# Optimization experiments

Hardware: AMD Instinct MI355X
Metric: run time of the kernel (lower is better)

Reference implementation:

```python
import jax, jax.numpy as jnp
import numpy as np

H = 8  # num_heads
EPS = 1e-5


def layer_norm(x, g, b):
    mu = jnp.mean(x, axis=-1, keepdims=True)
    var = jnp.mean((x - mu) ** 2, axis=-1, keepdims=True)
    return (x - mu) * jax.lax.rsqrt(var + EPS) * g + b


def setup_inputs() -> dict:
    key = jax.random.key(0)
    ks = jax.random.split(key, 8)
    B, N, C = 2, 2048, 512
    Dff = 2048
    s = 0.02
    x = jax.random.normal(ks[0], (B, N, C), dtype=jnp.float32)
    mask = (jax.random.uniform(ks[1], (N, N)) > 0.5).astype(jnp.float32)
    return {
        "x": x,
        "mask": mask,
        "w_qkv": jax.random.normal(ks[2], (3 * C, C), dtype=jnp.float32) * s,
        "w_proj": jax.random.normal(ks[3], (C, C), dtype=jnp.float32) * s,
        "b_proj": jnp.zeros((C,), jnp.float32),
        "g1": jnp.ones((C,), jnp.float32),
        "beta1": jnp.zeros((C,), jnp.float32),
        "g2": jnp.ones((C,), jnp.float32),
        "beta2": jnp.zeros((C,), jnp.float32),
        "w1": jax.random.normal(ks[4], (Dff, C), dtype=jnp.float32) * s,
        "bm1": jnp.zeros((Dff,), jnp.float32),
        "w2": jax.random.normal(ks[5], (C, Dff), dtype=jnp.float32) * s,
        "bm2": jnp.zeros((C,), jnp.float32),
    }


def attn_block(h, mask, w_qkv, w_proj, b_proj):
    B, N, C = h.shape
    hd = C // H
    scale = hd ** -0.5
    qkv = (h @ w_qkv.T).reshape(B, N, 3, H, hd)
    q, k, v = jnp.moveaxis(qkv, 2, 0)          # each [B, N, H, hd]
    q = q.transpose(0, 2, 1, 3)                 # [B, H, N, hd]
    k = k.transpose(0, 2, 1, 3)
    v = v.transpose(0, 2, 1, 3)
    attn = jnp.einsum("bhnd,bhmd->bhnm", q, k) * scale
    attn = attn * mask                          # multiplicative sparse mask
    attn = jax.nn.softmax(attn, axis=-1)
    o = jnp.einsum("bhnm,bhmd->bhnd", attn, v)
    o = o.transpose(0, 2, 1, 3).reshape(B, N, C)
    return o @ w_proj.T + b_proj


def reference(x, mask, w_qkv, w_proj, b_proj, g1, beta1, g2, beta2, w1, bm1, w2, bm2):
    # pre-norm transformer block, dropout/drop_path disabled (eval)
    y = x + attn_block(layer_norm(x, g1, beta1), mask, w_qkv, w_proj, b_proj)
    h = layer_norm(y, g2, beta2)
    h = jax.nn.gelu(h @ w1.T + bm1, approximate=False)  # torch F.gelu default (erf)
    z = y + (h @ w2.T + bm2)
    return z
```

## Files before the change

kernel.cpp:

```cpp
#include <hip/hip_runtime.h>
#include <cmath>
#include <stdint.h>

#define N_SEQ 2048
#define C_DIM 512
#define BATCH 2
#define NHEAD 8
#define DFF   2048
#define M_ROWS (BATCH * N_SEQ)

typedef unsigned short ushort_t;
typedef unsigned long long u64;
typedef __bf16 bf16x8 __attribute__((ext_vector_type(8)));
typedef float  f32x4  __attribute__((ext_vector_type(4)));
typedef float  f32x16 __attribute__((ext_vector_type(16)));

__device__ __forceinline__ float bf2f(ushort_t u) {
    union { unsigned int i; float f; } v; v.i = ((unsigned int)u) << 16; return v.f;
}
__device__ __forceinline__ ushort_t f2bf_(float f) {
    union { float f; unsigned int i; } v; v.f = f;
    unsigned int r = v.i + 0x7fffu + ((v.i >> 16) & 1u);
    return (ushort_t)(r >> 16);
}
__device__ __forceinline__ unsigned short bfbits(float f) {
    return __builtin_bit_cast(unsigned short, (__bf16)f);
}

__device__ __forceinline__ void load_lds16(const ushort_t* g, ushort_t* lds_wave_base) {
    __builtin_amdgcn_global_load_lds(
        (const __attribute__((address_space(1))) void*)g,
        (__attribute__((address_space(3))) void*)lds_wave_base, 16, 0, 0);
}

__global__ void probe_kernel(const unsigned int* __restrict__ g1w, int* __restrict__ flag) {
    if (threadIdx.x == 0 && blockIdx.x == 0)
        *flag = (g1w[0] == 0x3F800000u) ? 1 : 0;
}

__global__ __launch_bounds__(256) void convert_kernel(const int* __restrict__ flag,
        const void* w_qkv, const void* w_proj, const void* w1, const void* w2,
        ushort_t* wq_bf, ushort_t* wp_bf, ushort_t* w1_bf, ushort_t* w2_bf) {
    long e = ((long)blockIdx.x * 256 + threadIdx.x) * 8;
    const void* src; ushort_t* dst; long off;
    if      (e < 786432)  { src = w_qkv; dst = wq_bf;  off = e; }
    else if (e < 1048576) { src = w_proj; dst = wp_bf; off = e - 786432; }
    else if (e < 2097152) { src = w1;    dst = w1_bf;  off = e - 1048576; }
    else                  { src = w2;    dst = w2_bf;  off = e - 2097152; }
    bf16x8 r;
    if (*flag) {
        const float4* q = (const float4*)((const float*)src + off);
        float4 a = q[0], b = q[1];
        r[0]=(__bf16)a.x; r[1]=(__bf16)a.y; r[2]=(__bf16)a.z; r[3]=(__bf16)a.w;
        r[4]=(__bf16)b.x; r[5]=(__bf16)b.y; r[6]=(__bf16)b.z; r[7]=(__bf16)b.w;
    } else {
        r = *(const bf16x8*)((const ushort_t*)src + off);
    }
    *(bf16x8*)(dst + off) = r;
}

__global__ __launch_bounds__(256) void maskpack_kernel(const int* __restrict__ flag,
        const void* __restrict__ mask, u64* __restrict__ maskM) {
    int id = blockIdx.x * 256 + threadIdx.x;
    int q = id >> 5, kb = id & 31;
    int is32 = *flag;
    size_t base = (size_t)q * N_SEQ + kb * 64;
    u64 bits = 0;
    for (int j = 0; j < 64; ++j) {
        bool m = is32 ? (((const float*)mask)[base + j] != 0.0f)
                      : ((((const ushort_t*)mask)[base + j] & 0x7fffu) != 0);
        bits |= (u64)m << j;
    }
    maskM[(size_t)q * 32 + kb] = bits;
}

template <typename TX, typename TG>
__device__ __forceinline__ void ln_body(const TX* __restrict__ x, const TG* __restrict__ g,
                                        const TG* __restrict__ b, ushort_t* __restrict__ out) {
    int row  = blockIdx.x * 4 + (threadIdx.x >> 6);
    int lane = threadIdx.x & 63;
    const TX* xr = x + (size_t)row * C_DIM + lane * 8;
    float v[8];
    if (sizeof(TX) == 2) {
        bf16x8 t = *(const bf16x8*)xr;
        #pragma unroll
        for (int j = 0; j < 8; ++j) v[j] = (float)t[j];
    } else {
        const float4* q = (const float4*)xr;
        float4 a = q[0], c = q[1];
        v[0]=a.x; v[1]=a.y; v[2]=a.z; v[3]=a.w; v[4]=c.x; v[5]=c.y; v[6]=c.z; v[7]=c.w;
    }
    float s = 0.f, sq = 0.f;
    #pragma unroll
    for (int j = 0; j < 8; ++j) { s += v[j]; sq += v[j] * v[j]; }
    #pragma unroll
    for (int m = 1; m < 64; m <<= 1) { s += __shfl_xor(s, m, 64); sq += __shfl_xor(sq, m, 64); }
    float mean = s * (1.0f / C_DIM);
    float var  = fmaxf(sq * (1.0f / C_DIM) - mean * mean, 0.0f);
    float rs = rsqrtf(var + 1e-5f);
    float gv[8], bv[8];
    const TG* gp = g + lane * 8; const TG* bp = b + lane * 8;
    if (sizeof(TG) == 2) {
        bf16x8 tg = *(const bf16x8*)gp, tb = *(const bf16x8*)bp;
        #pragma unroll
        for (int j = 0; j < 8; ++j) { gv[j] = (float)tg[j]; bv[j] = (float)tb[j]; }
    } else {
        const float4* qg = (const float4*)gp; const float4* qb = (const float4*)bp;
        float4 a=qg[0], c=qg[1], d=qb[0], e=qb[1];
        gv[0]=a.x;gv[1]=a.y;gv[2]=a.z;gv[3]=a.w;gv[4]=c.x;gv[5]=c.y;gv[6]=c.z;gv[7]=c.w;
        bv[0]=d.x;bv[1]=d.y;bv[2]=d.z;bv[3]=d.w;bv[4]=e.x;bv[5]=e.y;bv[6]=e.z;bv[7]=e.w;
    }
    bf16x8 o;
    #pragma unroll
    for (int j = 0; j < 8; ++j) o[j] = (__bf16)((v[j] - mean) * rs * gv[j] + bv[j]);
    *(bf16x8*)(out + (size_t)row * C_DIM + lane * 8) = o;
}

__global__ __launch_bounds__(256) void ln1_kernel(const int* __restrict__ flag, const void* x,
                                                  const void* g, const void* b, ushort_t* out) {
    if (*flag) ln_body<float, float>((const float*)x, (const float*)g, (const float*)b, out);
    else       ln_body<ushort_t, ushort_t>((const ushort_t*)x, (const ushort_t*)g, (const ushort_t*)b, out);
}
__global__ __launch_bounds__(256) void ln2_kernel(const int* __restrict__ flag, const ushort_t* y,
                                                  const void* g, const void* b, ushort_t* out) {
    if (*flag) ln_body<ushort_t, float>(y, (const float*)g, (const float*)b, out);
    else       ln_body<ushort_t, ushort_t>(y, (const ushort_t*)g, (const ushort_t*)b, out);
}

template <int BN, int K, bool HAS_BIAS, int ACT, int RES_MODE, int OUT_MODE>
__global__ __launch_bounds__(256) void gemm_kernel(const int* __restrict__ flag,
        const ushort_t* __restrict__ A, const ushort_t* __restrict__ W,
        const void* __restrict__ bias, const void* __restrict__ res,
        void* __restrict__ Cout, int Nout) {
    constexpr int MT  = (BN == 128) ? 2 : 1;
    constexpr int RPW = (BN == 128) ? 32 : 16;
    __shared__ __align__(16) ushort_t As[64 * 32];
    __shared__ __align__(16) ushort_t Bs[BN * 32];
    int t = threadIdx.x;
    int wave = t >> 6, lane = t & 63, quad = lane >> 4, l16 = lane & 15;
    int wm = (BN == 128) ? (wave >> 1) : wave;
    int wn = (BN == 128) ? (wave & 1) : 0;
    int row0 = blockIdx.y * 64, col0 = blockIdx.x * BN;

    f32x4 acc[MT][4] = {};
    int arow = t >> 2, kofs = (t & 3) * 8;

    for (int k0 = 0; k0 < K; k0 += 32) {
        load_lds16(A + (size_t)(row0 + arow) * K + k0 + kofs, As + wave * 512);
        load_lds16(W + (size_t)(col0 + arow) * K + k0 + kofs, Bs + wave * 512);
        if (BN == 128)
            load_lds16(W + (size_t)(col0 + 64 + arow) * K + k0 + kofs, Bs + 2048 + wave * 512);
        __syncthreads();
        bf16x8 af[MT], bfr[4];
        #pragma unroll
        for (int i = 0; i < MT; ++i)
            af[i] = *(const bf16x8*)&As[(wm * RPW + i * 16 + l16) * 32 + quad * 8];
        #pragma unroll
        for (int j = 0; j < 4; ++j)
            bfr[j] = *(const bf16x8*)&Bs[(wn * 64 + j * 16 + l16) * 32 + quad * 8];
        #pragma unroll
        for (int i = 0; i < MT; ++i)
            #pragma unroll
            for (int j = 0; j < 4; ++j)
                acc[i][j] = __builtin_amdgcn_mfma_f32_16x16x32_bf16(af[i], bfr[j], acc[i][j], 0, 0, 0);
        __syncthreads();
    }

    int is32 = *flag;
    #pragma unroll
    for (int j = 0; j < 4; ++j) {
        int col = col0 + wn * 64 + j * 16 + l16;
        float bv = 0.0f;
        if (HAS_BIAS) bv = is32 ? ((const float*)bias)[col] : bf2f(((const ushort_t*)bias)[col]);
        #pragma unroll
        for (int i = 0; i < MT; ++i) {
            #pragma unroll
            for (int r = 0; r < 4; ++r) {
                int row = row0 + wm * RPW + i * 16 + quad * 4 + r;
                float v = acc[i][j][r] + bv;
                if (ACT == 1) v = 0.5f * v * (1.0f + erff(v * 0.70710678118654752f));
                size_t idx = (size_t)row * Nout + col;
                if (RES_MODE == 1) v += is32 ? ((const float*)res)[idx] : bf2f(((const ushort_t*)res)[idx]);
                if (RES_MODE == 3) v += bf2f(((const ushort_t*)res)[idx]);
                if (OUT_MODE == 0) ((ushort_t*)Cout)[idx] = f2bf_(v);
                else { if (is32) ((float*)Cout)[idx] = v; else ((ushort_t*)Cout)[idx] = f2bf_(v); }
            }
        }
    }
}

__global__ __launch_bounds__(128) void attn_kernel(
        const ushort_t* __restrict__ qkv, const u64* __restrict__ maskM,
        ushort_t* __restrict__ o0, ushort_t* __restrict__ o1,
        ushort_t* __restrict__ o2, ushort_t* __restrict__ o3,
        float* __restrict__ Lpart) {
    __shared__ __align__(16) ushort_t Ks[64][68];
    __shared__ __align__(16) ushort_t VTs[64][68];
    int t = threadIdx.x;
    int wave = t >> 6, lane = t & 63, l32 = lane & 31, H = lane >> 5;
    int qtile = blockIdx.x, bh = blockIdx.y, sp = blockIdx.z;
    int b = bh >> 3, h = bh & 7;
    int q = qtile * 64 + wave * 32 + l32;

    const ushort_t* base = qkv + (size_t)b * N_SEQ * 1536;
    const ushort_t* qp = base + h * 64;
    const ushort_t* kp = base + 512 + h * 64;
    const ushort_t* vp = base + 1024 + h * 64;

    bf16x8 bQ[4];
    #pragma unroll
    for (int c = 0; c < 4; ++c)
        bQ[c] = *(const bf16x8*)(qp + (size_t)q * 1536 + c * 16 + H * 8);

    int k_row = (t >> 3);
    int k_ch  = (t & 7) * 8;
    int v_kp0 = (t & 31) * 2;
    int v_db0 = (t >> 5) * 8;
    const int n_base = sp * 512;

    bf16x8 kreg[4], vreg[2][2];
    #pragma unroll
    for (int s = 0; s < 4; ++s)
        kreg[s] = *(const bf16x8*)(kp + (size_t)(n_base + s * 16 + k_row) * 1536 + k_ch);
    #pragma unroll
    for (int s = 0; s < 2; ++s)
        #pragma unroll
        for (int u = 0; u < 2; ++u)
            vreg[s][u] = *(const bf16x8*)(vp + (size_t)(n_base + v_kp0 + u) * 1536 + v_db0 + s * 32);
    u64 mw = maskM[(size_t)q * 32 + (n_base >> 6)];

    f32x16 o_acc[2] = {};
    float lsum = 0.0f;
    const float scale = 0.125f;

    for (int i = 0; i < 8; ++i) {
        int n0 = n_base + i * 64;
        __syncthreads();
        #pragma unroll
        for (int s = 0; s < 4; ++s)
            *(bf16x8*)&Ks[s * 16 + k_row][k_ch] = kreg[s];
        #pragma unroll
        for (int s = 0; s < 2; ++s)
            #pragma unroll
            for (int j = 0; j < 8; ++j) {
                unsigned int pair = (unsigned int)__builtin_bit_cast(unsigned short, vreg[s][0][j])
                                  | ((unsigned int)__builtin_bit_cast(unsigned short, vreg[s][1][j]) << 16);
                *(unsigned int*)&VTs[v_db0 + s * 32 + j][v_kp0] = pair;
            }
        __syncthreads();
        if (i < 7) {
            int n1 = n0 + 64;
            #pragma unroll
            for (int s = 0; s < 4; ++s)
                kreg[s] = *(const bf16x8*)(kp + (size_t)(n1 + s * 16 + k_row) * 1536 + k_ch);
            #pragma unroll
            for (int s = 0; s < 2; ++s)
                #pragma unroll
                for (int u = 0; u < 2; ++u)
                    vreg[s][u] = *(const bf16x8*)(vp + (size_t)(n1 + v_kp0 + u) * 1536 + v_db0 + s * 32);
        }
        f32x16 s_acc[2] = {};
        #pragma unroll
        for (int kt = 0; kt < 2; ++kt)
            #pragma unroll
            for (int c = 0; c < 4; ++c) {
                bf16x8 aK = *(const bf16x8*)&Ks[kt * 32 + l32][c * 16 + H * 8];
                s_acc[kt] = __builtin_amdgcn_mfma_f32_32x32x16_bf16(aK, bQ[c], s_acc[kt], 0, 0, 0);
            }
        unsigned int P2[2][8];
        #pragma unroll
        for (int kt = 0; kt < 2; ++kt) {
            float p[16];
            #pragma unroll
            for (int r = 0; r < 16; ++r) {
                int keyloc = kt * 32 + (r & 3) + 8 * (r >> 2) + 4 * H;
                float e = __expf(s_acc[kt][r] * scale);
                p[r] = ((mw >> keyloc) & 1) ? e : 1.0f;
                lsum += p[r];
            }
            #pragma unroll
            for (int pr = 0; pr < 8; ++pr)
                P2[kt][pr] = (unsigned int)bfbits(p[2 * pr])
                           | ((unsigned int)bfbits(p[2 * pr + 1]) << 16);
        }
        if (i < 7) mw = maskM[(size_t)q * 32 + ((n0 + 64) >> 6)];
        unsigned int rv[2][4];
        #pragma unroll
        for (int kt = 0; kt < 2; ++kt)
            #pragma unroll
            for (int u = 0; u < 4; ++u) {
                int idx = (u & 1) + (u >> 1) * 4;
                unsigned int send = H ? P2[kt][idx] : P2[kt][idx + 2];
                rv[kt][u] = (unsigned int)__shfl_xor((int)send, 32, 64);
            }
        #pragma unroll
        for (int kc = 0; kc < 4; ++kc) {
            const int kt = kc >> 1, klo = kc & 1;
            union { unsigned int w[4]; bf16x8 v; } bP;
            #pragma unroll
            for (int w = 0; w < 4; ++w) {
                unsigned int own = H ? P2[kt][(w & 1) + 4 * klo + 2] : P2[kt][(w & 1) + 4 * klo];
                unsigned int oth = rv[kt][(w & 1) + 2 * klo];
                bP.w[w] = ((w >> 1) == H) ? own : oth;
            }
            #pragma unroll
            for (int dt = 0; dt < 2; ++dt) {
                bf16x8 aV = *(const bf16x8*)&VTs[dt * 32 + l32][kc * 16 + H * 8];
                o_acc[dt] = __builtin_amdgcn_mfma_f32_32x32x16_bf16(aV, bP.v, o_acc[dt], 0, 0, 0);
            }
        }
    }
    lsum += __shfl_xor(lsum, 32, 64);
    ushort_t* osel = (sp == 0) ? o0 : (sp == 1) ? o1 : (sp == 2) ? o2 : o3;
    ushort_t* op = osel + (size_t)bh * N_SEQ * 64;
    #pragma unroll
    for (int dt = 0; dt < 2; ++dt)
        #pragma unroll
        for (int r4 = 0; r4 < 4; ++r4) {
            int d = dt * 32 + 8 * r4 + 4 * H;
            ushort4 val;
            val.x = f2bf_(o_acc[dt][r4 * 4 + 0]);
            val.y = f2bf_(o_acc[dt][r4 * 4 + 1]);
            val.z = f2bf_(o_acc[dt][r4 * 4 + 2]);
            val.w = f2bf_(o_acc[dt][r4 * 4 + 3]);
            *(ushort4*)&op[(size_t)q * 64 + d] = val;
        }
    if (H == 0)
        Lpart[((size_t)sp * 16 + bh) * N_SEQ + q] = lsum;
}

__global__ __launch_bounds__(256) void combine_kernel(
        const ushort_t* __restrict__ o0, const ushort_t* __restrict__ o1,
        const ushort_t* __restrict__ o2, const ushort_t* __restrict__ o3,
        const float* __restrict__ Lpart, ushort_t* __restrict__ attno) {
    int gid = blockIdx.x * 256 + threadIdx.x;
    int rowg = gid >> 4;
    int dq = (gid & 15) * 4;
    int bh = rowg >> 11, qq = rowg & 2047, b = bh >> 3, h = bh & 7;
    const ushort_t* ops[4] = { o0, o1, o2, o3 };
    float acc[4] = {};
    float l = 0.0f;
    #pragma unroll
    for (int sp = 0; sp < 4; ++sp) {
        ushort4 o = *(const ushort4*)&ops[sp][(size_t)rowg * 64 + dq];
        acc[0] += bf2f(o.x); acc[1] += bf2f(o.y); acc[2] += bf2f(o.z); acc[3] += bf2f(o.w);
        l += Lpart[(size_t)sp * 16 * N_SEQ + rowg];
    }
    float inv = 1.0f / l;
    ushort4 res;
    res.x = f2bf_(acc[0] * inv); res.y = f2bf_(acc[1] * inv);
    res.z = f2bf_(acc[2] * inv); res.w = f2bf_(acc[3] * inv);
    *(ushort4*)&attno[((size_t)b * N_SEQ + qq) * C_DIM + h * 64 + dq] = res;
}

extern "C" void kernel_launch(void* const* d_in, const int* in_sizes, int n_in,
                              void* d_out, int out_size, void* d_ws, size_t ws_size,
                              hipStream_t stream) {
    char* ws = (char*)d_ws;
    const size_t KB = 1024;
    int*      flag  = (int*)ws;
    ushort_t* wq_bf = (ushort_t*)(ws + 256 * KB);
    ushort_t* wp_bf = (ushort_t*)(ws + 1792 * KB);
    ushort_t* w1_bf = (ushort_t*)(ws + 2304 * KB);
    ushort_t* w2_bf = (ushort_t*)(ws + 4352 * KB);
    u64*      maskM = (u64*)     (ws + 6400 * KB);
    ushort_t* h     = (ushort_t*)(ws + 6912 * KB);
    ushort_t* attno = (ushort_t*)(ws + 11008 * KB);
    ushort_t* y     = (ushort_t*)(ws + 15104 * KB);
    ushort_t* qkv   = (ushort_t*)(ws + 19200 * KB);
    ushort_t* Op2   = (ushort_t*)(ws + 31488 * KB);
    ushort_t* Op3   = (ushort_t*)(ws + 35584 * KB);
    float*    Lpart = (float*)   (ws + 39680 * KB);
    ushort_t* Op0   = h;
    ushort_t* Op1   = y;
    ushort_t* gmid  = (ushort_t*)(ws + 19200 * KB);

    probe_kernel<<<1, 64, 0, stream>>>((const unsigned int*)d_in[5], flag);
    convert_kernel<<<1536, 256, 0, stream>>>(flag, d_in[2], d_in[3], d_in[9], d_in[11],
                                             wq_bf, wp_bf, w1_bf, w2_bf);
    maskpack_kernel<<<256, 256, 0, stream>>>(flag, d_in[1], maskM);
    ln1_kernel<<<M_ROWS / 4, 256, 0, stream>>>(flag, d_in[0], d_in[5], d_in[6], h);
    gemm_kernel<128, 512, false, 0, 0, 0><<<dim3(1536 / 128, 64), 256, 0, stream>>>(
        flag, h, wq_bf, nullptr, nullptr, qkv, 1536);
    attn_kernel<<<dim3(N_SEQ / 64, BATCH * NHEAD, 4), 128, 0, stream>>>(
        qkv, maskM, Op0, Op1, Op2, Op3, Lpart);
    combine_kernel<<<2048, 256, 0, stream>>>(Op0, Op1, Op2, Op3, Lpart, attno);
    gemm_kernel<64, 512, true, 0, 1, 0><<<dim3(C_DIM / 64, 64), 256, 0, stream>>>(
        flag, attno, wp_bf, d_in[4], d_in[0], y, C_DIM);
    ln2_kernel<<<M_ROWS / 4, 256, 0, stream>>>(flag, y, d_in[7], d_in[8], h);
    gemm_kernel<128, 512, true, 1, 0, 0><<<dim3(DFF / 128, 64), 256, 0, stream>>>(
        flag, h, w1_bf, d_in[10], nullptr, gmid, DFF);
    gemm_kernel<64, 2048, true, 0, 3, 2><<<dim3(C_DIM / 64, 64), 256, 0, stream>>>(
        flag, gmid, w2_bf, d_in[12], y, d_out, C_DIM);
}
```

Baseline: 263.1 us.

## Fuse prep kernels, fold split-K combine into proj GEMM, enlarge attention tiles

Merges the probe, weight convert, mask pack and LN1 kernels into one prep launch, and packs the mask with wave ballots instead of a serial per-thread loop. The split-attention combine moves into the projection GEMM's A-tile load, which removes the intermediate attno buffer and a launch. The attention kernel now runs 256 threads per block over 128 queries, and pre-scales Q by scale*log2e so it can use exp2f. The costs are redundant partial-sum and reciprocal work on every K-step of the proj GEMM, and a register-staged A load in place of the direct global-to-LDS load.

Measured after the change: 352.8 us. 34.1% more time.

```diff
diff --git a/kernel.cpp b/kernel.cpp
--- a/kernel.cpp
+++ b/kernel.cpp
@@ -26,6 +26,9 @@
 __device__ __forceinline__ unsigned short bfbits(float f) {
     return __builtin_bit_cast(unsigned short, (__bf16)f);
 }
+__device__ __forceinline__ int get_is32(const unsigned int* g1w) {
+    return g1w[0] == 0x3F800000u;
+}
 
 __device__ __forceinline__ void load_lds16(const ushort_t* g, ushort_t* lds_wave_base) {
     __builtin_amdgcn_global_load_lds(
@@ -33,52 +36,10 @@
         (__attribute__((address_space(3))) void*)lds_wave_base, 16, 0, 0);
 }
 
-__global__ void probe_kernel(const unsigned int* __restrict__ g1w, int* __restrict__ flag) {
-    if (threadIdx.x == 0 && blockIdx.x == 0)
-        *flag = (g1w[0] == 0x3F800000u) ? 1 : 0;
-}
-
-__global__ __launch_bounds__(256) void convert_kernel(const int* __restrict__ flag,
-        const void* w_qkv, const void* w_proj, const void* w1, const void* w2,
-        ushort_t* wq_bf, ushort_t* wp_bf, ushort_t* w1_bf, ushort_t* w2_bf) {
-    long e = ((long)blockIdx.x * 256 + threadIdx.x) * 8;
-    const void* src; ushort_t* dst; long off;
-    if      (e < 786432)  { src = w_qkv; dst = wq_bf;  off = e; }
-    else if (e < 1048576) { src = w_proj; dst = wp_bf; off = e - 786432; }
-    else if (e < 2097152) { src = w1;    dst = w1_bf;  off = e - 1048576; }
-    else                  { src = w2;    dst = w2_bf;  off = e - 2097152; }
-    bf16x8 r;
-    if (*flag) {
-        const float4* q = (const float4*)((const float*)src + off);
-        float4 a = q[0], b = q[1];
-        r[0]=(__bf16)a.x; r[1]=(__bf16)a.y; r[2]=(__bf16)a.z; r[3]=(__bf16)a.w;
-        r[4]=(__bf16)b.x; r[5]=(__bf16)b.y; r[6]=(__bf16)b.z; r[7]=(__bf16)b.w;
-    } else {
-        r = *(const bf16x8*)((const ushort_t*)src + off);
-    }
-    *(bf16x8*)(dst + off) = r;
-}
-
-__global__ __launch_bounds__(256) void maskpack_kernel(const int* __restrict__ flag,
-        const void* __restrict__ mask, u64* __restrict__ maskM) {
-    int id = blockIdx.x * 256 + threadIdx.x;
-    int q = id >> 5, kb = id & 31;
-    int is32 = *flag;
-    size_t base = (size_t)q * N_SEQ + kb * 64;
-    u64 bits = 0;
-    for (int j = 0; j < 64; ++j) {
-        bool m = is32 ? (((const float*)mask)[base + j] != 0.0f)
-                      : ((((const ushort_t*)mask)[base + j] & 0x7fffu) != 0);
-        bits |= (u64)m << j;
-    }
-    maskM[(size_t)q * 32 + kb] = bits;
-}
-
 template <typename TX, typename TG>
-__device__ __forceinline__ void ln_body(const TX* __restrict__ x, const TG* __restrict__ g,
-                                        const TG* __restrict__ b, ushort_t* __restrict__ out) {
-    int row  = blockIdx.x * 4 + (threadIdx.x >> 6);
-    int lane = threadIdx.x & 63;
+__device__ __forceinline__ void ln_row(int row, int lane, const TX* __restrict__ x,
+                                       const TG* __restrict__ g, const TG* __restrict__ b,
+                                       ushort_t* __restrict__ out) {
     const TX* xr = x + (size_t)row * C_DIM + lane * 8;
     float v[8];
     if (sizeof(TX) == 2) {
@@ -116,19 +77,59 @@
     *(bf16x8*)(out + (size_t)row * C_DIM + lane * 8) = o;
 }
 
-__global__ __launch_bounds__(256) void ln1_kernel(const int* __restrict__ flag, const void* x,
-                                                  const void* g, const void* b, ushort_t* out) {
-    if (*flag) ln_body<float, float>((const float*)x, (const float*)g, (const float*)b, out);
-    else       ln_body<ushort_t, ushort_t>((const ushort_t*)x, (const ushort_t*)g, (const ushort_t*)b, out);
-}
-__global__ __launch_bounds__(256) void ln2_kernel(const int* __restrict__ flag, const ushort_t* y,
-                                                  const void* g, const void* b, ushort_t* out) {
-    if (*flag) ln_body<ushort_t, float>(y, (const float*)g, (const float*)b, out);
-    else       ln_body<ushort_t, ushort_t>(y, (const ushort_t*)g, (const ushort_t*)b, out);
+__global__ __launch_bounds__(256) void prep_kernel(const unsigned int* __restrict__ g1w,
+        const void* w_qkv, const void* w_proj, const void* w1, const void* w2,
+        const void* mask, const void* x, const void* g1, const void* b1,
+        ushort_t* wq_bf, ushort_t* wp_bf, ushort_t* w1_bf, ushort_t* w2_bf,
+        u64* __restrict__ maskM, ushort_t* __restrict__ hout) {
+    int is32 = get_is32(g1w);
+    int bid = blockIdx.x;
+    int wave = threadIdx.x >> 6, lane = threadIdx.x & 63;
+    if (bid < 1536) {
+        long e = ((long)bid * 256 + threadIdx.x) * 8;
+        const void* src; ushort_t* dst; long off;
+        if      (e < 786432)  { src = w_qkv; dst = wq_bf;  off = e; }
+        else if (e < 1048576) { src = w_proj; dst = wp_bf; off = e - 786432; }
+        else if (e < 2097152) { src = w1;    dst = w1_bf;  off = e - 1048576; }
+        else                  { src = w2;    dst = w2_bf;  off = e - 2097152; }
+        bf16x8 r;
+        if (is32) {
+            const float4* q = (const float4*)((const float*)src + off);
+            float4 a = q[0], b = q[1];
+            r[0]=(__bf16)a.x; r[1]=(__bf16)a.y; r[2]=(__bf16)a.z; r[3]=(__bf16)a.w;
+            r[4]=(__bf16)b.x; r[5]=(__bf16)b.y; r[6]=(__bf16)b.z; r[7]=(__bf16)b.w;
+        } else {
+            r = *(const bf16x8*)((const ushort_t*)src + off);
+        }
+        *(bf16x8*)(dst + off) = r;
+    } else if (bid < 2560) {
+        int pb = bid - 1536;
+        #pragma unroll
+        for (int it = 0; it < 16; ++it) {
+            int p = pb * 64 + wave * 16 + it;
+            int q = p >> 5, kb = p & 31;
+            size_t idx = (size_t)q * N_SEQ + kb * 64 + lane;
+            bool m = is32 ? (((const float*)mask)[idx] != 0.0f)
+                          : ((((const ushort_t*)mask)[idx] & 0x7fffu) != 0);
+            u64 bits = __ballot(m);
+            if (lane == 0) maskM[(size_t)q * 32 + kb] = bits;
+        }
+    } else {
+        int row = (bid - 2560) * 4 + wave;
+        if (is32) ln_row<float, float>(row, lane, (const float*)x, (const float*)g1, (const float*)b1, hout);
+        else      ln_row<ushort_t, ushort_t>(row, lane, (const ushort_t*)x, (const ushort_t*)g1, (const ushort_t*)b1, hout);
+    }
+}
+
+__global__ __launch_bounds__(256) void ln2_kernel(const unsigned int* __restrict__ g1w,
+        const ushort_t* __restrict__ y, const void* g, const void* b, ushort_t* out) {
+    int row = blockIdx.x * 4 + (threadIdx.x >> 6), lane = threadIdx.x & 63;
+    if (get_is32(g1w)) ln_row<ushort_t, float>(row, lane, y, (const float*)g, (const float*)b, out);
+    else               ln_row<ushort_t, ushort_t>(row, lane, y, (const ushort_t*)g, (const ushort_t*)b, out);
 }
 
 template <int BN, int K, bool HAS_BIAS, int ACT, int RES_MODE, int OUT_MODE>
-__global__ __launch_bounds__(256) void gemm_kernel(const int* __restrict__ flag,
+__global__ __launch_bounds__(256) void gemm_kernel(const unsigned int* __restrict__ g1w,
         const ushort_t* __restrict__ A, const ushort_t* __restrict__ W,
         const void* __restrict__ bias, const void* __restrict__ res,
         void* __restrict__ Cout, int Nout) {
@@ -166,7 +167,7 @@
         __syncthreads();
     }
 
-    int is32 = *flag;
+    int is32 = get_is32(g1w);
     #pragma unroll
     for (int j = 0; j < 4; ++j) {
         int col = col0 + wn * 64 + j * 16 + l16;
@@ -180,7 +181,6 @@
                 float v = acc[i][j][r] + bv;
                 if (ACT == 1) v = 0.5f * v * (1.0f + erff(v * 0.70710678118654752f));
                 size_t idx = (size_t)row * Nout + col;
-                if (RES_MODE == 1) v += is32 ? ((const float*)res)[idx] : bf2f(((const ushort_t*)res)[idx]);
                 if (RES_MODE == 3) v += bf2f(((const ushort_t*)res)[idx]);
                 if (OUT_MODE == 0) ((ushort_t*)Cout)[idx] = f2bf_(v);
                 else { if (is32) ((float*)Cout)[idx] = v; else ((ushort_t*)Cout)[idx] = f2bf_(v); }
@@ -189,7 +189,68 @@
     }
 }
 
-__global__ __launch_bounds__(128) void attn_kernel(
+__global__ __launch_bounds__(256) void proj_gemm_kernel(const unsigned int* __restrict__ g1w,
+        const ushort_t* __restrict__ o0, const ushort_t* __restrict__ o1,
+        const ushort_t* __restrict__ o2, const ushort_t* __restrict__ o3,
+        const float* __restrict__ Lpart,
+        const ushort_t* __restrict__ W, const void* __restrict__ bias,
+        const void* __restrict__ res, ushort_t* __restrict__ Cout) {
+    __shared__ __align__(16) ushort_t As[64 * 32];
+    __shared__ __align__(16) ushort_t Bs[64 * 32];
+    int t = threadIdx.x;
+    int wave = t >> 6, lane = t & 63, quad = lane >> 4, l16 = lane & 15;
+    int row0 = blockIdx.y * 64, col0 = blockIdx.x * 64;
+
+    f32x4 acc[4] = {};
+    int arow = t >> 2, kofs = (t & 3) * 8;
+    int row_t = row0 + arow;
+    int b_ = row_t >> 11, q_ = row_t & 2047;
+
+    for (int k0 = 0; k0 < 512; k0 += 32) {
+        int k = k0 + kofs;
+        int hh = k >> 6, d = k & 63;
+        size_t rowg = (size_t)(b_ * 8 + hh) * 2048 + q_;
+        float l = Lpart[rowg] + Lpart[32768 + rowg] + Lpart[65536 + rowg] + Lpart[98304 + rowg];
+        float inv = 1.0f / l;
+        const ushort_t* p0 = o0 + rowg * 64 + d;
+        const ushort_t* p1 = o1 + rowg * 64 + d;
+        const ushort_t* p2 = o2 + rowg * 64 + d;
+        const ushort_t* p3 = o3 + rowg * 64 + d;
+        bf16x8 av;
+        #pragma unroll
+        for (int j = 0; j < 8; ++j) {
+            float s = bf2f(p0[j]) + bf2f(p1[j]) + bf2f(p2[j]) + bf2f(p3[j]);
+            av[j] = (__bf16)(s * inv);
+        }
+        *(bf16x8*)&As[arow * 32 + kofs] = av;
+        load_lds16(W + (size_t)(col0 + arow) * 512 + k0 + kofs, Bs + wave * 512);
+        __syncthreads();
+        bf16x8 af = *(const bf16x8*)&As[(wave * 16 + l16) * 32 + quad * 8];
+        #pragma unroll
+        for (int j = 0; j < 4; ++j) {
+            bf16x8 bfr = *(const bf16x8*)&Bs[(j * 16 + l16) * 32 + quad * 8];
+            acc[j] = __builtin_amdgcn_mfma_f32_16x16x32_bf16(af, bfr, acc[j], 0, 0, 0);
+        }
+        __syncthreads();
+    }
+
+    int is32 = get_is32(g1w);
+    #pragma unroll
+    for (int j = 0; j < 4; ++j) {
+        int col = col0 + j * 16 + l16;
+        float bv = is32 ? ((const float*)bias)[col] : bf2f(((const ushort_t*)bias)[col]);
+        #pragma unroll
+        for (int r = 0; r < 4; ++r) {
+            int row = row0 + wave * 16 + quad * 4 + r;
+            size_t idx = (size_t)row * C_DIM + col;
+            float v = acc[j][r] + bv;
+            v += is32 ? ((const float*)res)[idx] : bf2f(((const ushort_t*)res)[idx]);
+            Cout[idx] = f2bf_(v);
+        }
+    }
+}
+
+__global__ __launch_bounds__(256, 4) void attn_kernel(
         const ushort_t* __restrict__ qkv, const u64* __restrict__ maskM,
         ushort_t* __restrict__ o0, ushort_t* __restrict__ o1,
         ushort_t* __restrict__ o2, ushort_t* __restrict__ o3,
@@ -200,64 +261,59 @@
     int wave = t >> 6, lane = t & 63, l32 = lane & 31, H = lane >> 5;
     int qtile = blockIdx.x, bh = blockIdx.y, sp = blockIdx.z;
     int b = bh >> 3, h = bh & 7;
-    int q = qtile * 64 + wave * 32 + l32;
+    int q = qtile * 128 + wave * 32 + l32;
 
     const ushort_t* base = qkv + (size_t)b * N_SEQ * 1536;
     const ushort_t* qp = base + h * 64;
     const ushort_t* kp = base + 512 + h * 64;
     const ushort_t* vp = base + 1024 + h * 64;
 
+    const float qs = 0.125f * 1.44269504088896f;
     bf16x8 bQ[4];
     #pragma unroll
-    for (int c = 0; c < 4; ++c)
-        bQ[c] = *(const bf16x8*)(qp + (size_t)q * 1536 + c * 16 + H * 8);
-
-    int k_row = (t >> 3);
-    int k_ch  = (t & 7) * 8;
-    int v_kp0 = (t & 31) * 2;
-    int v_db0 = (t >> 5) * 8;
+    for (int c = 0; c < 4; ++c) {
+        bf16x8 raw = *(const bf16x8*)(qp + (size_t)q * 1536 + c * 16 + H * 8);
+        #pragma unroll
+        for (int j = 0; j < 8; ++j) bQ[c][j] = (__bf16)((float)raw[j] * qs);
+    }
+
+    int k_r = t >> 3, k_ch = (t & 7) * 8;
+    int v_kp = (t & 31) * 2, v_db = (t >> 5) * 8;
     const int n_base = sp * 512;
 
-    bf16x8 kreg[4], vreg[2][2];
-    #pragma unroll
-    for (int s = 0; s < 4; ++s)
-        kreg[s] = *(const bf16x8*)(kp + (size_t)(n_base + s * 16 + k_row) * 1536 + k_ch);
+    bf16x8 kreg[2], vreg[2];
     #pragma unroll
     for (int s = 0; s < 2; ++s)
-        #pragma unroll
-        for (int u = 0; u < 2; ++u)
-            vreg[s][u] = *(const bf16x8*)(vp + (size_t)(n_base + v_kp0 + u) * 1536 + v_db0 + s * 32);
+        kreg[s] = *(const bf16x8*)(kp + (size_t)(n_base + s * 32 + k_r) * 1536 + k_ch);
+    #pragma unroll
+    for (int u = 0; u < 2; ++u)
+        vreg[u] = *(const bf16x8*)(vp + (size_t)(n_base + v_kp + u) * 1536 + v_db);
     u64 mw = maskM[(size_t)q * 32 + (n_base >> 6)];
 
     f32x16 o_acc[2] = {};
     float lsum = 0.0f;
-    const float scale = 0.125f;
 
     for (int i = 0; i < 8; ++i) {
         int n0 = n_base + i * 64;
         __syncthreads();
         #pragma unroll
-        for (int s = 0; s < 4; ++s)
-            *(bf16x8*)&Ks[s * 16 + k_row][k_ch] = kreg[s];
-        #pragma unroll
         for (int s = 0; s < 2; ++s)
-            #pragma unroll
-            for (int j = 0; j < 8; ++j) {
-                unsigned int pair = (unsigned int)__builtin_bit_cast(unsigned short, vreg[s][0][j])
-                                  | ((unsigned int)__builtin_bit_cast(unsigned short, vreg[s][1][j]) << 16);
-                *(unsigned int*)&VTs[v_db0 + s * 32 + j][v_kp0] = pair;
-            }
+            *(bf16x8*)&Ks[s * 32 + k_r][k_ch] = kreg[s];
+        #pragma unroll
+        for (int j = 0; j < 8; ++j) {
+            unsigned int pair = (unsigned int)__builtin_bit_cast(unsigned short, vreg[0][j])
+                              | ((unsigned int)__builtin_bit_cast(unsigned short, vreg[1][j]) << 16);
+            *(unsigned int*)&VTs[v_db + j][v_kp] = pair;
+        }
         __syncthreads();
         if (i < 7) {
             int n1 = n0 + 64;
             #pragma unroll
-            for (int s = 0; s < 4; ++s)
-                kreg[s] = *(const bf16x8*)(kp + (size_t)(n1 + s * 16 + k_row) * 1536 + k_ch);
-            #pragma unroll
             for (int s = 0; s < 2; ++s)
-                #pragma unroll
-                for (int u = 0; u < 2; ++u)
-                    vreg[s][u] = *(const bf16x8*)(vp + (size_t)(n1 + v_kp0 + u) * 1536 + v_db0 + s * 32);
+                kreg[s] = *(const bf16x8*)(kp + (size_t)(n1 + s * 32 + k_r) * 1536 + k_ch);
+            #pragma unroll
+            for (int u = 0; u < 2; ++u)
+                vreg[u] = *(const bf16x8*)(vp + (size_t)(n1 + v_kp + u) * 1536 + v_db);
         }
         f32x16 s_acc[2] = {};
         #pragma unroll
@@ -274,7 +330,7 @@
             #pragma unroll
             for (int r = 0; r < 16; ++r) {
                 int keyloc = kt * 32 + (r & 3) + 8 * (r >> 2) + 4 * H;
-                float e = __expf(s_acc[kt][r] * scale);
+                float e = exp2f(s_acc[kt][r]);
                 p[r] = ((mw >> keyloc) & 1) ? e : 1.0f;
                 lsum += p[r];
             }
@@ -329,67 +385,39 @@
         Lpart[((size_t)sp * 16 + bh) * N_SEQ + q] = lsum;
 }
 
-__global__ __launch_bounds__(256) void combine_kernel(
-        const ushort_t* __restrict__ o0, const ushort_t* __restrict__ o1,
-        const ushort_t* __restrict__ o2, const ushort_t* __restrict__ o3,
-        const float* __restrict__ Lpart, ushort_t* __restrict__ attno) {
-    int gid = blockIdx.x * 256 + threadIdx.x;
-    int rowg = gid >> 4;
-    int dq = (gid & 15) * 4;
-    int bh = rowg >> 11, qq = rowg & 2047, b = bh >> 3, h = bh & 7;
-    const ushort_t* ops[4] = { o0, o1, o2, o3 };
-    float acc[4] = {};
-    float l = 0.0f;
-    #pragma unroll
-    for (int sp = 0; sp < 4; ++sp) {
-        ushort4 o = *(const ushort4*)&ops[sp][(size_t)rowg * 64 + dq];
-        acc[0] += bf2f(o.x); acc[1] += bf2f(o.y); acc[2] += bf2f(o.z); acc[3] += bf2f(o.w);
-        l += Lpart[(size_t)sp * 16 * N_SEQ + rowg];
-    }
-    float inv = 1.0f / l;
-    ushort4 res;
-    res.x = f2bf_(acc[0] * inv); res.y = f2bf_(acc[1] * inv);
-    res.z = f2bf_(acc[2] * inv); res.w = f2bf_(acc[3] * inv);
-    *(ushort4*)&attno[((size_t)b * N_SEQ + qq) * C_DIM + h * 64 + dq] = res;
-}
-
 extern "C" void kernel_launch(void* const* d_in, const int* in_sizes, int n_in,
                               void* d_out, int out_size, void* d_ws, size_t ws_size,
                               hipStream_t stream) {
     char* ws = (char*)d_ws;
     const size_t KB = 1024;
-    int*      flag  = (int*)ws;
-    ushort_t* wq_bf = (ushort_t*)(ws + 256 * KB);
-    ushort_t* wp_bf = (ushort_t*)(ws + 1792 * KB);
-    ushort_t* w1_bf = (ushort_t*)(ws + 2304 * KB);
-    ushort_t* w2_bf = (ushort_t*)(ws + 4352 * KB);
-    u64*      maskM = (u64*)     (ws + 6400 * KB);
-    ushort_t* h     = (ushort_t*)(ws + 6912 * KB);
-    ushort_t* attno = (ushort_t*)(ws + 11008 * KB);
-    ushort_t* y     = (ushort_t*)(ws + 15104 * KB);
-    ushort_t* qkv   = (ushort_t*)(ws + 19200 * KB);
-    ushort_t* Op2   = (ushort_t*)(ws + 31488 * KB);
-    ushort_t* Op3   = (ushort_t*)(ws + 35584 * KB);
-    float*    Lpart = (float*)   (ws + 39680 * KB);
-    ushort_t* Op0   = h;
-    ushort_t* Op1   = y;
-    ushort_t* gmid  = (ushort_t*)(ws + 19200 * KB);
-
-    probe_kernel<<<1, 64, 0, stream>>>((const unsigned int*)d_in[5], flag);
-    convert_kernel<<<1536, 256, 0, stream>>>(flag, d_in[2], d_in[3], d_in[9], d_in[11],
-                                             wq_bf, wp_bf, w1_bf, w2_bf);
-    maskpack_kernel<<<256, 256, 0, stream>>>(flag, d_in[1], maskM);
-    ln1_kernel<<<M_ROWS / 4, 256, 0, stream>>>(flag, d_in[0], d_in[5], d_in[6], h);
+    const unsigned int* g1w = (const unsigned int*)d_in[5];
+    ushort_t* wq_bf = (ushort_t*)(ws);
+    ushort_t* wp_bf = (ushort_t*)(ws + 1536 * KB);
+    ushort_t* w1_bf = (ushort_t*)(ws + 2048 * KB);
+    ushort_t* w2_bf = (ushort_t*)(ws + 4096 * KB);
+    u64*      maskM = (u64*)     (ws + 6144 * KB);
+    ushort_t* h     = (ushort_t*)(ws + 6656 * KB);
+    ushort_t* y     = (ushort_t*)(ws + 10752 * KB);
+    ushort_t* qkv   = (ushort_t*)(ws + 14848 * KB);
+    ushort_t* Op0   = (ushort_t*)(ws + 27136 * KB);
+    ushort_t* Op1   = (ushort_t*)(ws + 31232 * KB);
+    ushort_t* Op2   = (ushort_t*)(ws + 35328 * KB);
+    ushort_t* Op3   = (ushort_t*)(ws + 39424 * KB);
+    float*    Lpart = (float*)   (ws + 43520 * KB);
+    ushort_t* gmid  = (ushort_t*)(ws + 14848 * KB);
+
+    prep_kernel<<<3584, 256, 0, stream>>>(g1w, d_in[2], d_in[3], d_in[9], d_in[11],
+                                          d_in[1], d_in[0], d_in[5], d_in[6],
+                                          wq_bf, wp_bf, w1_bf, w2_bf, maskM, h);
     gemm_kernel<128, 512, false, 0, 0, 0><<<dim3(1536 / 128, 64), 256, 0, stream>>>(
-        flag, h, wq_bf, nullptr, nullptr, qkv, 1536);
-    attn_kernel<<<dim3(N_SEQ / 64, BATCH * NHEAD, 4), 128, 0, stream>>>(
+        g1w, h, wq_bf, nullptr, nullptr, qkv, 1536);
+    attn_kernel<<<dim3(N_SEQ / 128, BATCH * NHEAD, 4), 256, 0, stream>>>(
         qkv, maskM, Op0, Op1, Op2, Op3, Lpart);
-    combine_kernel<<<2048, 256, 0, stream>>>(Op0, Op1, Op2, Op3, Lpart, attno);
-    gemm_kernel<64, 512, true, 0, 1, 0><<<dim3(C_DIM / 64, 64), 256, 0, stream>>>(
-        flag, attno, wp_bf, d_in[4], d_in[0], y, C_DIM);
-    ln2_kernel<<<M_ROWS / 4, 256, 0, stream>>>(flag, y, d_in[7], d_in[8], h);
+    proj_gemm_kernel<<<dim3(C_DIM / 64, 64), 256, 0, stream>>>(
+        g1w, Op0, Op1, Op2, Op3, Lpart, wp_bf, d_in[4], d_in[0], y);
+    ln2_kernel<<<M_ROWS / 4, 256, 0, stream>>>(g1w, y, d_in[7], d_in[8], h);
     gemm_kernel<128, 512, true, 1, 0, 0><<<dim3(DFF / 128, 64), 256, 0, stream>>>(
-        flag, h, w1_bf, d_in[10], nullptr, gmid, DFF);
+        g1w, h, w1_bf, d_in[10], nullptr, gmid, DFF);
     gemm_kernel<64, 2048, true, 0, 3, 2><<<dim3(C_DIM / 64, 64), 256, 0, stream>>>(
-        flag, gmid, w2_bf, d_in[12], y, d_out, C_DIM);
-}
+        g1w, gmid, w2_bf, d_in[12], y, d_out, C_DIM);
+}
```
